# Optimization experiments

Measured on AMD Instinct MI355X. Metric: run time of the kernel, lower is better.

## Reference

```python
import jax, jax.numpy as jnp
import numpy as np

B, S, D, FF, V, H, M = 4, 512, 768, 3072, 30000, 12, 64
DH = D // H
N_LAYERS = 12  # shared ALBERT layer applied 12 times


def _positional_encoding():
    pos = jnp.arange(S, dtype=jnp.float32)[:, None]                      # [S,1]
    denom = jnp.power(10000.0, 2.0 * jnp.arange(D, dtype=jnp.float32) / D)
    pe = pos / denom                                                     # [S,D]
    pe = pe.at[1:, 0::2].set(jnp.sin(pe[1:, 0::2]))
    pe = pe.at[1:, 1::2].set(jnp.cos(pe[1:, 1::2]))
    return pe


def setup_inputs() -> dict:
    key = jax.random.key(0)
    ks = jax.random.split(key, 20)
    tok = jax.random.randint(ks[0], (B, S), 0, V)
    texts_onehot = jax.nn.one_hot(tok, V, dtype=jnp.float32)
    w = lambda k, shp: (jax.random.normal(k, shp, jnp.float32) * 0.02)
    return {
        'texts_onehot': texts_onehot,
        'se_w': w(ks[1], (V, D)), 'se_b': w(ks[2], (D,)),
        'wq': w(ks[3], (D, D)), 'bq': w(ks[4], (D,)),
        'wk': w(ks[5], (D, D)), 'bk': w(ks[6], (D,)),
        'wv': w(ks[7], (D, D)), 'bv': w(ks[8], (D,)),
        'wo': w(ks[9], (D, D)), 'bo': w(ks[10], (D,)),
        'w1': w(ks[11], (D, FF)), 'b1': w(ks[12], (FF,)),
        'w2': w(ks[13], (FF, D)), 'b2': w(ks[14], (D,)),
        'we': w(ks[15], (D, V)), 'be': w(ks[16], (V,)),
        'idx': jax.random.randint(ks[17], (B, M), 0, S),
    }


def _layernorm(x):
    mean = jnp.mean(x, axis=-1, keepdims=True)
    var = jnp.mean(jnp.square(x - mean), axis=-1, keepdims=True)
    return (x - mean) / jnp.sqrt(var + 1e-5)


def reference(texts_onehot, se_w, se_b, wq, bq, wk, bk, wv, bv, wo, bo,
              w1, b1, w2, b2, we, be, idx):
    pe = _positional_encoding()                                          # [S,D]
    x = texts_onehot @ se_w + se_b + pe                                  # [B,S,D]
    scale = 1.0 / jnp.sqrt(jnp.float32(DH))

    def mha(x):
        q = (x @ wq + bq).reshape(B, S, H, DH)
        k = (x @ wk + bk).reshape(B, S, H, DH)
        v = (x @ wv + bv).reshape(B, S, H, DH)
        att = jax.nn.softmax(jnp.einsum('bqhd,bkhd->bhqk', q, k) * scale, axis=-1)
        o = jnp.einsum('bhqk,bkhd->bqhd', att, v).reshape(B, S, D)
        return o @ wo + bo

    for _ in range(N_LAYERS):  # same (shared) weights every iteration
        x = _layernorm(x + mha(x))
        x = jax.nn.relu(x @ w1 + b1) @ w2 + b2

    # gather masked positions then project to vocab + log_softmax
    g = jnp.take_along_axis(x, idx[..., None], axis=1)                   # [B,M,D]
    logits = g @ we + be                                                 # [B,M,V]
    return jax.nn.log_softmax(logits, axis=-1).reshape(B * M, V)
```

## Files before the change

kernel.cpp:

```cpp
#include <hip/hip_runtime.h>
#include <hip/hip_bf16.h>
#include <math.h>

#define Bv 4
#define Sv 512
#define Dv 768
#define FFv 3072
#define Vv 30000
#define Vpad 30080
#define Hv 12
#define Mv 64
#define DHv 64
#define NLAYERS 12
#define QKVN 2304

typedef __attribute__((ext_vector_type(8))) short short8;
typedef __attribute__((ext_vector_type(4))) float floatx4;

static __device__ __forceinline__ short f2b(float f) {
  union { float f; unsigned u; } v; v.f = f;
  unsigned r = v.u + 0x7fffu + ((v.u >> 16) & 1u);
  return (short)(r >> 16);
}

#define GLD16(gp, lp) __builtin_amdgcn_global_load_lds( \
    (__attribute__((address_space(1))) void*)(gp), \
    (__attribute__((address_space(3))) void*)(lp), 16, 0, 0)

__global__ __launch_bounds__(256) void transpose_w(
    const float* __restrict__ W, short* __restrict__ Wt,
    int K, int N, int Nout)
{
  __shared__ float t[32][33];
  int n0 = blockIdx.x * 32, k0 = blockIdx.y * 32;
  int tx = threadIdx.x & 31, ty = threadIdx.x >> 5;
  #pragma unroll
  for (int i = 0; i < 4; i++) {
    int k = k0 + ty + i * 8, n = n0 + tx;
    t[ty + i * 8][tx] = (n < N) ? W[(size_t)k * N + n] : 0.f;
  }
  __syncthreads();
  #pragma unroll
  for (int i = 0; i < 4; i++) {
    int n = n0 + ty + i * 8, k = k0 + tx;
    if (n < Nout) Wt[(size_t)n * K + k] = f2b(t[tx][ty + i * 8]);
  }
}

__global__ __launch_bounds__(256) void pack_bias(
    const float* __restrict__ bq, const float* __restrict__ bk,
    const float* __restrict__ bv, float* __restrict__ bqkv)
{
  int i = blockIdx.x * 256 + threadIdx.x;
  if (i < Dv) { bqkv[i] = bq[i]; bqkv[Dv + i] = bk[i]; bqkv[2 * Dv + i] = bv[i]; }
}

__global__ __launch_bounds__(256) void embed_kernel(
    const float* __restrict__ oh, const float* __restrict__ sew,
    const float* __restrict__ seb, float* __restrict__ xf,
    short* __restrict__ xb)
{
  int bs = blockIdx.x;
  int s = bs & (Sv - 1);
  __shared__ int tokS;
  const float* row = oh + (size_t)bs * Vv;
  for (int j = threadIdx.x * 4; j < Vv; j += 256 * 4) {
    float4 f = *(const float4*)(row + j);
    if (f.x != 0.f) tokS = j;
    if (f.y != 0.f) tokS = j + 1;
    if (f.z != 0.f) tokS = j + 2;
    if (f.w != 0.f) tokS = j + 3;
  }
  __syncthreads();
  int tok = tokS;
  for (int d = threadIdx.x; d < Dv; d += 256) {
    float pe = 0.f;
    if (s > 0) {
      float denom = expf(9.210340371976184f * (2.f * (float)d / 768.f));
      float raw = (float)s / denom;
      pe = (d & 1) ? cosf(raw) : sinf(raw);
    }
    float val = sew[(size_t)tok * Dv + d] + seb[d] + pe;
    xf[(size_t)bs * Dv + d] = val;
    xb[(size_t)bs * Dv + d] = f2b(val);
  }
}

template <int BM, int BN, int WM, int WN>
__global__ __launch_bounds__(256) void gemm_bt(
    const short* __restrict__ A, const short* __restrict__ Bt,
    const float* __restrict__ bias, float* __restrict__ Cf,
    short* __restrict__ Cb, int M, int N, int K, int relu)
{
  __shared__ __align__(16) short As[BM * 64];
  __shared__ __align__(16) short Bs[BN * 64];
  int n0 = blockIdx.x * BN, m0 = blockIdx.y * BM;
  int tid = threadIdx.x;
  int wave = tid >> 6, lane = tid & 63, quad = lane >> 4, l16 = lane & 15;
  int wm = (wave >> 1) * WM, wn = (wave & 1) * WN;

  floatx4 acc[WM / 16][WN / 16];
  #pragma unroll
  for (int i = 0; i < WM / 16; i++)
    #pragma unroll
    for (int j = 0; j < WN / 16; j++) acc[i][j] = (floatx4){0.f, 0.f, 0.f, 0.f};

  int srow[4], skc[4];
  #pragma unroll
  for (int it = 0; it < 4; it++) {
    int c = it * 256 + tid;
    srow[it] = c >> 3;
    skc[it] = (c & 7) ^ (srow[it] & 7);
  }

  for (int k0 = 0; k0 < K; k0 += 64) {
    __syncthreads();
    #pragma unroll
    for (int it = 0; it < BM / 32; it++)
      GLD16(A + (size_t)(m0 + srow[it]) * K + k0 + skc[it] * 8,
            As + (it * 2048 + wave * 512));
    #pragma unroll
    for (int it = 0; it < BN / 32; it++)
      GLD16(Bt + (size_t)(n0 + srow[it]) * K + k0 + skc[it] * 8,
            Bs + (it * 2048 + wave * 512));
    __syncthreads();
    #pragma unroll
    for (int kh = 0; kh < 2; kh++) {
      short8 af[WM / 16], bfr[WN / 16];
      int kc = kh * 4 + quad;
      #pragma unroll
      for (int i = 0; i < WM / 16; i++) {
        int ra = wm + i * 16 + l16;
        af[i] = *(const short8*)(As + (ra * 8 + (kc ^ (ra & 7))) * 8);
      }
      #pragma unroll
      for (int j = 0; j < WN / 16; j++) {
        int rb = wn + j * 16 + l16;
        bfr[j] = *(const short8*)(Bs + (rb * 8 + (kc ^ (rb & 7))) * 8);
      }
      #pragma unroll
      for (int i = 0; i < WM / 16; i++)
        #pragma unroll
        for (int j = 0; j < WN / 16; j++)
          acc[i][j] = __builtin_amdgcn_mfma_f32_16x16x32_bf16(af[i], bfr[j], acc[i][j], 0, 0, 0);
    }
  }

  #pragma unroll
  for (int i = 0; i < WM / 16; i++) {
    int row = m0 + wm + i * 16 + quad * 4;
    #pragma unroll
    for (int j = 0; j < WN / 16; j++) {
      int col = n0 + wn + j * 16 + l16;
      if (col < N) {
        float bb = bias ? bias[col] : 0.f;
        #pragma unroll
        for (int r = 0; r < 4; r++) {
          float val = acc[i][j][r] + bb;
          if (relu) val = fmaxf(val, 0.f);
          size_t off = (size_t)(row + r) * N + col;
          if (Cf) Cf[off] = val;
          if (Cb) Cb[off] = f2b(val);
        }
      }
    }
  }
}

__global__ __launch_bounds__(256) void attn_fused(
    const short* __restrict__ qkv, short* __restrict__ O)
{
  __shared__ __align__(16) short lv[64][40];
  __shared__ __align__(16) short pbuf[4][16][40];
  int q0 = blockIdx.x * 64;
  int bh = blockIdx.y;
  int b = bh / Hv, h = bh - b * Hv;
  int tid = threadIdx.x;
  int wave = tid >> 6, lane = tid & 63, quad = lane >> 4, l16 = lane & 15;

  floatx4 acc[32];
  #pragma unroll
  for (int c = 0; c < 32; c++) acc[c] = (floatx4){0.f, 0.f, 0.f, 0.f};

  const short* Qrow = qkv + (size_t)(b * Sv + q0 + wave * 16 + l16) * QKVN + h * DHv;
  short8 a0 = *(const short8*)(Qrow + quad * 8);
  short8 a1 = *(const short8*)(Qrow + 32 + quad * 8);
  const short* Kbase = qkv + Dv + (size_t)(b * Sv + l16) * QKVN + h * DHv + quad * 8;
  #pragma unroll
  for (int c = 0; c < 32; c++) {
    const short* Kp = Kbase + (size_t)c * 16 * QKVN;
    short8 b0 = *(const short8*)(Kp);
    short8 b1 = *(const short8*)(Kp + 32);
    acc[c] = __builtin_amdgcn_mfma_f32_16x16x32_bf16(a0, b0, acc[c], 0, 0, 0);
    acc[c] = __builtin_amdgcn_mfma_f32_16x16x32_bf16(a1, b1, acc[c], 0, 0, 0);
  }

  float inv[4];
  #pragma unroll
  for (int r = 0; r < 4; r++) {
    float m = -1e30f;
    #pragma unroll
    for (int c = 0; c < 32; c++) m = fmaxf(m, acc[c][r]);
    m = fmaxf(m, __shfl_xor(m, 1));
    m = fmaxf(m, __shfl_xor(m, 2));
    m = fmaxf(m, __shfl_xor(m, 4));
    m = fmaxf(m, __shfl_xor(m, 8));
    float s = 0.f;
    #pragma unroll
    for (int c = 0; c < 32; c++) {
      float e = __expf((acc[c][r] - m) * 0.125f);
      acc[c][r] = e; s += e;
    }
    s += __shfl_xor(s, 1);
    s += __shfl_xor(s, 2);
    s += __shfl_xor(s, 4);
    s += __shfl_xor(s, 8);
    inv[r] = 1.f / s;
  }

  floatx4 acc_o[4];
  #pragma unroll
  for (int j = 0; j < 4; j++) acc_o[j] = (floatx4){0.f, 0.f, 0.f, 0.f};

  const short* Vbase = qkv + 2 * Dv + h * DHv + (size_t)(b * Sv) * QKVN;
  for (int kc = 0; kc < 16; kc++) {
    __syncthreads();
    #pragma unroll
    for (int i = 0; i < 4; i++) {
      int u = i * 256 + tid;
      int kk = u >> 5, nn2 = (u & 31) * 2;
      const short* vp = Vbase + (size_t)(kc * 32 + kk) * QKVN + nn2;
      short v0 = vp[0], v1 = vp[1];
      lv[nn2][kk] = v0;
      lv[nn2 + 1][kk] = v1;
    }
    #pragma unroll
    for (int half = 0; half < 2; half++) {
      int c = 2 * kc + half;
      #pragma unroll
      for (int r = 0; r < 4; r++)
        pbuf[wave][quad * 4 + r][half * 16 + l16] = f2b(acc[c][r] * inv[r]);
    }
    __syncthreads();
    short8 af = *(const short8*)(&pbuf[wave][l16][quad * 8]);
    #pragma unroll
    for (int j = 0; j < 4; j++) {
      short8 bf = *(const short8*)(&lv[j * 16 + l16][quad * 8]);
      acc_o[j] = __builtin_amdgcn_mfma_f32_16x16x32_bf16(af, bf, acc_o[j], 0, 0, 0);
    }
  }

  int row = q0 + wave * 16 + quad * 4;
  #pragma unroll
  for (int j = 0; j < 4; j++) {
    int col = h * DHv + j * 16 + l16;
    #pragma unroll
    for (int r = 0; r < 4; r++)
      O[(size_t)(b * Sv + row + r) * Dv + col] = f2b(acc_o[j][r]);
  }
}

__global__ __launch_bounds__(256) void addln_kernel(
    float* __restrict__ xf, const float* __restrict__ mh,
    short* __restrict__ xb)
{
  int r = blockIdx.x, t = threadIdx.x;
  size_t base = (size_t)r * Dv;
  float v[3];
  #pragma unroll
  for (int i = 0; i < 3; i++) {
    int d = t + i * 256;
    v[i] = xf[base + d] + mh[base + d];
  }
  __shared__ float red[256];
  red[t] = v[0] + v[1] + v[2];
  __syncthreads();
  for (int s2 = 128; s2 > 0; s2 >>= 1) { if (t < s2) red[t] += red[t + s2]; __syncthreads(); }
  float mean = red[0] * (1.f / 768.f);
  __syncthreads();
  float sq = 0.f;
  #pragma unroll
  for (int i = 0; i < 3; i++) { float d2 = v[i] - mean; sq += d2 * d2; }
  red[t] = sq;
  __syncthreads();
  for (int s2 = 128; s2 > 0; s2 >>= 1) { if (t < s2) red[t] += red[t + s2]; __syncthreads(); }
  float inv = rsqrtf(red[0] * (1.f / 768.f) + 1e-5f);
  #pragma unroll
  for (int i = 0; i < 3; i++) {
    int d = t + i * 256;
    float o = (v[i] - mean) * inv;
    xf[base + d] = o;
    xb[base + d] = f2b(o);
  }
}

__global__ __launch_bounds__(256) void gather_kernel(
    const short* __restrict__ xb, const int* __restrict__ idx,
    short* __restrict__ g)
{
  int bm = blockIdx.x;
  int b = bm >> 6;
  int s = idx[bm];
  for (int d = threadIdx.x; d < Dv; d += 256)
    g[(size_t)bm * Dv + d] = xb[(size_t)(b * Sv + s) * Dv + d];
}

__global__ __launch_bounds__(256) void lsm_kernel(
    const float* __restrict__ L, float* __restrict__ out)
{
  int r = blockIdx.x, t = threadIdx.x;
  const float* p = L + (size_t)r * Vv;
  float m = -1e30f;
  for (int j = t; j < Vv; j += 256) m = fmaxf(m, p[j]);
  __shared__ float red[256];
  red[t] = m;
  __syncthreads();
  for (int s2 = 128; s2 > 0; s2 >>= 1) { if (t < s2) red[t] = fmaxf(red[t], red[t + s2]); __syncthreads(); }
  m = red[0];
  __syncthreads();
  float s = 0.f;
  for (int j = t; j < Vv; j += 256) s += expf(p[j] - m);
  red[t] = s;
  __syncthreads();
  for (int s2 = 128; s2 > 0; s2 >>= 1) { if (t < s2) red[t] += red[t + s2]; __syncthreads(); }
  float lse = m + logf(red[0]);
  for (int j = t; j < Vv; j += 256) out[(size_t)r * Vv + j] = p[j] - lse;
}

extern "C" void kernel_launch(void* const* d_in, const int* in_sizes, int n_in,
                              void* d_out, int out_size, void* d_ws, size_t ws_size,
                              hipStream_t stream) {
  const float* oh  = (const float*)d_in[0];
  const float* sew = (const float*)d_in[1];
  const float* seb = (const float*)d_in[2];
  const float* wq  = (const float*)d_in[3];  const float* bq = (const float*)d_in[4];
  const float* wk  = (const float*)d_in[5];  const float* bk = (const float*)d_in[6];
  const float* wv  = (const float*)d_in[7];  const float* bv = (const float*)d_in[8];
  const float* wo  = (const float*)d_in[9];  const float* bo = (const float*)d_in[10];
  const float* w1  = (const float*)d_in[11]; const float* b1 = (const float*)d_in[12];
  const float* w2  = (const float*)d_in[13]; const float* b2 = (const float*)d_in[14];
  const float* we  = (const float*)d_in[15]; const float* be = (const float*)d_in[16];
  const int*   idx = (const int*)d_in[17];
  float* out = (float*)d_out;

  char* p = (char*)d_ws;
  auto alloc = [&](size_t bytes) -> char* {
    char* r = p; p += (bytes + 255) & ~(size_t)255; return r;
  };
  const size_t BS = (size_t)Bv * Sv;
  short* wqkv_t = (short*)alloc((size_t)QKVN * Dv * 2);
  short* wo_t   = (short*)alloc((size_t)Dv * Dv * 2);
  short* w1_t   = (short*)alloc((size_t)FFv * Dv * 2);
  short* w2_t   = (short*)alloc((size_t)Dv * FFv * 2);
  float* bqkv   = (float*)alloc(QKVN * 4);
  short* xb     = (short*)alloc(BS * Dv * 2);
  float* xf     = (float*)alloc(BS * Dv * 4);
  short* g      = (short*)alloc((size_t)Bv * Mv * Dv * 2);
  char*  TR     = p;
  short* qkv   = (short*)TR;
  short* o     = (short*)(TR + ((BS * QKVN * 2 + 255) & ~(size_t)255));
  float* mh    = (float*)((char*)o + ((BS * Dv * 2 + 255) & ~(size_t)255));
  short* t1    = (short*)((char*)mh + ((BS * Dv * 4 + 255) & ~(size_t)255));
  short* we_t = (short*)TR;
  float* lg   = (float*)(TR + (((size_t)Vpad * Dv * 2 + 255) & ~(size_t)255));

  transpose_w<<<dim3(24, 24), 256, 0, stream>>>(wq, wqkv_t,            Dv, Dv, Dv);
  transpose_w<<<dim3(24, 24), 256, 0, stream>>>(wk, wqkv_t + Dv * Dv,  Dv, Dv, Dv);
  transpose_w<<<dim3(24, 24), 256, 0, stream>>>(wv, wqkv_t + 2*Dv*Dv,  Dv, Dv, Dv);
  transpose_w<<<dim3(24, 24), 256, 0, stream>>>(wo, wo_t,              Dv, Dv, Dv);
  transpose_w<<<dim3(96, 24), 256, 0, stream>>>(w1, w1_t,              Dv, FFv, FFv);
  transpose_w<<<dim3(24, 96), 256, 0, stream>>>(w2, w2_t,              FFv, Dv, Dv);
  pack_bias<<<3, 256, 0, stream>>>(bq, bk, bv, bqkv);

  embed_kernel<<<(int)BS, 256, 0, stream>>>(oh, sew, seb, xf, xb);

  dim3 gQKV(QKVN / 128, (int)BS / 128);
  dim3 gD64(Dv / 64, (int)BS / 64);
  dim3 gFF(FFv / 128, (int)BS / 128);
  for (int l = 0; l < NLAYERS; l++) {
    gemm_bt<128,128,64,64><<<gQKV, 256, 0, stream>>>(xb, wqkv_t, bqkv, nullptr, qkv, (int)BS, QKVN, Dv, 0);
    attn_fused<<<dim3(Sv / 64, Bv * Hv), 256, 0, stream>>>(qkv, o);
    gemm_bt<64,64,32,32><<<gD64, 256, 0, stream>>>(o, wo_t, bo, mh, nullptr, (int)BS, Dv, Dv, 0);
    addln_kernel<<<(int)BS, 256, 0, stream>>>(xf, mh, xb);
    gemm_bt<128,128,64,64><<<gFF, 256, 0, stream>>>(xb, w1_t, b1, nullptr, t1, (int)BS, FFv, Dv, 1);
    gemm_bt<64,64,32,32><<<gD64, 256, 0, stream>>>(t1, w2_t, b2, xf, xb, (int)BS, Dv, FFv, 0);
  }

  transpose_w<<<dim3(940, 24), 256, 0, stream>>>(we, we_t, Dv, Vv, Vpad);
  gather_kernel<<<Bv * Mv, 256, 0, stream>>>(xb, idx, g);
  gemm_bt<128,128,64,64><<<dim3(Vpad / 128, (Bv * Mv) / 128), 256, 0, stream>>>(
      g, we_t, be, lg, nullptr, Bv * Mv, Vv, Dv, 0);
  lsm_kernel<<<Bv * Mv, 256, 0, stream>>>(lg, out);
}
```

Before: 2.421 ms.

## Preload full V tile into LDS during QK, add workgroup remap and BK template

The attention kernel now stages the whole 512x64 V slice into a swizzled 64 KB LDS buffer. The global loads are interleaved with the QK^T MFMA loop, which removes the 32 per-chunk barriers in the PV loop. Both the GEMM and attention kernels remap workgroup IDs in groups of 8, presumably to improve L2/XCD locality. The GEMM gains a BK template parameter, and the 64x64 tiles now use BK=128 to halve the number of k-iterations. The large LDS allocation lowers attention occupancy, and the extra live V registers raise register pressure.

```diff
diff --git a/kernel.cpp b/kernel.cpp
--- a/kernel.cpp
+++ b/kernel.cpp
@@ -86,15 +86,25 @@
   }
 }
 
-template <int BM, int BN, int WM, int WN>
+template <int BM, int BN, int WM, int WN, int BK>
 __global__ __launch_bounds__(256) void gemm_bt(
     const short* __restrict__ A, const short* __restrict__ Bt,
     const float* __restrict__ bias, float* __restrict__ Cf,
     short* __restrict__ Cb, int M, int N, int K, int relu)
 {
-  __shared__ __align__(16) short As[BM * 64];
-  __shared__ __align__(16) short Bs[BN * 64];
-  int n0 = blockIdx.x * BN, m0 = blockIdx.y * BM;
+  constexpr int CPR = BK / 8;
+  constexpr int ITA = BM * BK / 2048;
+  constexpr int ITB = BN * BK / 2048;
+  constexpr int ITMAX = ITA > ITB ? ITA : ITB;
+  __shared__ __align__(16) short As[BM * BK];
+  __shared__ __align__(16) short Bs[BN * BK];
+
+  int nwgx = gridDim.x;
+  int nwg = nwgx * gridDim.y;
+  int fid = blockIdx.y * nwgx + blockIdx.x;
+  if ((nwg & 7) == 0) fid = (fid & 7) * (nwg >> 3) + (fid >> 3);
+  int n0 = (fid % nwgx) * BN, m0 = (fid / nwgx) * BM;
+
   int tid = threadIdx.x;
   int wave = tid >> 6, lane = tid & 63, quad = lane >> 4, l16 = lane & 15;
   int wm = (wave >> 1) * WM, wn = (wave & 1) * WN;
@@ -105,38 +115,38 @@
     #pragma unroll
     for (int j = 0; j < WN / 16; j++) acc[i][j] = (floatx4){0.f, 0.f, 0.f, 0.f};
 
-  int srow[4], skc[4];
-  #pragma unroll
-  for (int it = 0; it < 4; it++) {
+  int srow[ITMAX], skc[ITMAX];
+  #pragma unroll
+  for (int it = 0; it < ITMAX; it++) {
     int c = it * 256 + tid;
-    srow[it] = c >> 3;
-    skc[it] = (c & 7) ^ (srow[it] & 7);
-  }
-
-  for (int k0 = 0; k0 < K; k0 += 64) {
+    srow[it] = c / CPR;
+    skc[it] = (c & (CPR - 1)) ^ (srow[it] & 7);
+  }
+
+  for (int k0 = 0; k0 < K; k0 += BK) {
     __syncthreads();
     #pragma unroll
-    for (int it = 0; it < BM / 32; it++)
+    for (int it = 0; it < ITA; it++)
       GLD16(A + (size_t)(m0 + srow[it]) * K + k0 + skc[it] * 8,
             As + (it * 2048 + wave * 512));
     #pragma unroll
-    for (int it = 0; it < BN / 32; it++)
+    for (int it = 0; it < ITB; it++)
       GLD16(Bt + (size_t)(n0 + srow[it]) * K + k0 + skc[it] * 8,
             Bs + (it * 2048 + wave * 512));
     __syncthreads();
     #pragma unroll
-    for (int kh = 0; kh < 2; kh++) {
+    for (int kh = 0; kh < BK / 32; kh++) {
       short8 af[WM / 16], bfr[WN / 16];
       int kc = kh * 4 + quad;
       #pragma unroll
       for (int i = 0; i < WM / 16; i++) {
         int ra = wm + i * 16 + l16;
-        af[i] = *(const short8*)(As + (ra * 8 + (kc ^ (ra & 7))) * 8);
+        af[i] = *(const short8*)(As + (ra * CPR + (kc ^ (ra & 7))) * 8);
       }
       #pragma unroll
       for (int j = 0; j < WN / 16; j++) {
         int rb = wn + j * 16 + l16;
-        bfr[j] = *(const short8*)(Bs + (rb * 8 + (kc ^ (rb & 7))) * 8);
+        bfr[j] = *(const short8*)(Bs + (rb * CPR + (kc ^ (rb & 7))) * 8);
       }
       #pragma unroll
       for (int i = 0; i < WM / 16; i++)
@@ -170,10 +180,13 @@
 __global__ __launch_bounds__(256) void attn_fused(
     const short* __restrict__ qkv, short* __restrict__ O)
 {
-  __shared__ __align__(16) short lv[64][40];
+  __shared__ __align__(16) short lv[64 * 512];
   __shared__ __align__(16) short pbuf[4][16][40];
-  int q0 = blockIdx.x * 64;
-  int bh = blockIdx.y;
+
+  int fid = blockIdx.y * gridDim.x + blockIdx.x;
+  fid = (fid & 7) * 48 + (fid >> 3);
+  int q0 = (fid & 7) * 64;
+  int bh = fid >> 3;
   int b = bh / Hv, h = bh - b * Hv;
   int tid = threadIdx.x;
   int wave = tid >> 6, lane = tid & 63, quad = lane >> 4, l16 = lane & 15;
@@ -186,13 +199,40 @@
   short8 a0 = *(const short8*)(Qrow + quad * 8);
   short8 a1 = *(const short8*)(Qrow + 32 + quad * 8);
   const short* Kbase = qkv + Dv + (size_t)(b * Sv + l16) * QKVN + h * DHv + quad * 8;
-  #pragma unroll
-  for (int c = 0; c < 32; c++) {
-    const short* Kp = Kbase + (size_t)c * 16 * QKVN;
-    short8 b0 = *(const short8*)(Kp);
-    short8 b1 = *(const short8*)(Kp + 32);
-    acc[c] = __builtin_amdgcn_mfma_f32_16x16x32_bf16(a0, b0, acc[c], 0, 0, 0);
-    acc[c] = __builtin_amdgcn_mfma_f32_16x16x32_bf16(a1, b1, acc[c], 0, 0, 0);
+  const short* Vbase = qkv + 2 * Dv + h * DHv + (size_t)(b * Sv) * QKVN;
+
+  int kb_t = tid >> 5;
+  int n2_t = (tid & 31) * 2;
+  short2 vreg[16];
+
+#define LOADQ(qi) do { \
+    _Pragma("unroll") \
+    for (int i = 0; i < 16; i++) { \
+      int kk = (qi) * 128 + i * 8 + kb_t; \
+      vreg[i] = *(const short2*)(Vbase + (size_t)kk * QKVN + n2_t); \
+    } } while (0)
+#define WRITEQ(qi) do { \
+    _Pragma("unroll") \
+    for (int i = 0; i < 16; i++) { \
+      int ch = (qi) * 16 + i; \
+      int sw0 = (ch & ~7) | ((ch ^ n2_t) & 7); \
+      lv[n2_t * 512 + sw0 * 8 + kb_t] = vreg[i].x; \
+      lv[(n2_t + 1) * 512 + (sw0 ^ 1) * 8 + kb_t] = vreg[i].y; \
+    } } while (0)
+
+  #pragma unroll
+  for (int g = 0; g < 4; g++) {
+    if (g > 0) WRITEQ(g - 1);
+    LOADQ(g);
+    #pragma unroll
+    for (int cc = 0; cc < 8; cc++) {
+      int c = g * 8 + cc;
+      const short* Kp = Kbase + (size_t)c * 16 * QKVN;
+      short8 b0 = *(const short8*)(Kp);
+      short8 b1 = *(const short8*)(Kp + 32);
+      acc[c] = __builtin_amdgcn_mfma_f32_16x16x32_bf16(a0, b0, acc[c], 0, 0, 0);
+      acc[c] = __builtin_amdgcn_mfma_f32_16x16x32_bf16(a1, b1, acc[c], 0, 0, 0);
+    }
   }
 
   float inv[4];
@@ -218,22 +258,15 @@
     inv[r] = 1.f / s;
   }
 
+  WRITEQ(3);
+  __syncthreads();
+
   floatx4 acc_o[4];
   #pragma unroll
   for (int j = 0; j < 4; j++) acc_o[j] = (floatx4){0.f, 0.f, 0.f, 0.f};
 
-  const short* Vbase = qkv + 2 * Dv + h * DHv + (size_t)(b * Sv) * QKVN;
+  #pragma unroll
   for (int kc = 0; kc < 16; kc++) {
-    __syncthreads();
-    #pragma unroll
-    for (int i = 0; i < 4; i++) {
-      int u = i * 256 + tid;
-      int kk = u >> 5, nn2 = (u & 31) * 2;
-      const short* vp = Vbase + (size_t)(kc * 32 + kk) * QKVN + nn2;
-      short v0 = vp[0], v1 = vp[1];
-      lv[nn2][kk] = v0;
-      lv[nn2 + 1][kk] = v1;
-    }
     #pragma unroll
     for (int half = 0; half < 2; half++) {
       int c = 2 * kc + half;
@@ -241,14 +274,18 @@
       for (int r = 0; r < 4; r++)
         pbuf[wave][quad * 4 + r][half * 16 + l16] = f2b(acc[c][r] * inv[r]);
     }
-    __syncthreads();
     short8 af = *(const short8*)(&pbuf[wave][l16][quad * 8]);
     #pragma unroll
     for (int j = 0; j < 4; j++) {
-      short8 bf = *(const short8*)(&lv[j * 16 + l16][quad * 8]);
+      int n = j * 16 + l16;
+      int ch = kc * 4 + quad;
+      int sw = (ch & ~7) | ((ch ^ n) & 7);
+      short8 bf = *(const short8*)(lv + n * 512 + sw * 8);
       acc_o[j] = __builtin_amdgcn_mfma_f32_16x16x32_bf16(af, bf, acc_o[j], 0, 0, 0);
     }
   }
+#undef LOADQ
+#undef WRITEQ
 
   int row = q0 + wave * 16 + quad * 4;
   #pragma unroll
@@ -378,17 +415,17 @@
   dim3 gD64(Dv / 64, (int)BS / 64);
   dim3 gFF(FFv / 128, (int)BS / 128);
   for (int l = 0; l < NLAYERS; l++) {
-    gemm_bt<128,128,64,64><<<gQKV, 256, 0, stream>>>(xb, wqkv_t, bqkv, nullptr, qkv, (int)BS, QKVN, Dv, 0);
+    gemm_bt<128,128,64,64,64><<<gQKV, 256, 0, stream>>>(xb, wqkv_t, bqkv, nullptr, qkv, (int)BS, QKVN, Dv, 0);
     attn_fused<<<dim3(Sv / 64, Bv * Hv), 256, 0, stream>>>(qkv, o);
-    gemm_bt<64,64,32,32><<<gD64, 256, 0, stream>>>(o, wo_t, bo, mh, nullptr, (int)BS, Dv, Dv, 0);
+    gemm_bt<64,64,32,32,128><<<gD64, 256, 0, stream>>>(o, wo_t, bo, mh, nullptr, (int)BS, Dv, Dv, 0);
     addln_kernel<<<(int)BS, 256, 0, stream>>>(xf, mh, xb);
-    gemm_bt<128,128,64,64><<<gFF, 256, 0, stream>>>(xb, w1_t, b1, nullptr, t1, (int)BS, FFv, Dv, 1);
-    gemm_bt<64,64,32,32><<<gD64, 256, 0, stream>>>(t1, w2_t, b2, xf, xb, (int)BS, Dv, FFv, 0);
+    gemm_bt<128,128,64,64,64><<<gFF, 256, 0, stream>>>(xb, w1_t, b1, nullptr, t1, (int)BS, FFv, Dv, 1);
+    gemm_bt<64,64,32,32,128><<<gD64, 256, 0, stream>>>(t1, w2_t, b2, xf, xb, (int)BS, Dv, FFv, 0);
   }
 
   transpose_w<<<dim3(940, 24), 256, 0, stream>>>(we, we_t, Dv, Vv, Vpad);
   gather_kernel<<<Bv * Mv, 256, 0, stream>>>(xb, idx, g);
-  gemm_bt<128,128,64,64><<<dim3(Vpad / 128, (Bv * Mv) / 128), 256, 0, stream>>>(
+  gemm_bt<128,128,64,64,64><<<dim3(Vpad / 128, (Bv * Mv) / 128), 256, 0, stream>>>(
       g, we_t, be, lg, nullptr, Bv * Mv, Vv, Dv, 0);
   lsm_kernel<<<Bv * Mv, 256, 0, stream>>>(lg, out);
 }
```

Result: faster. 2.055 ms (-15.1%).
